# Kernel tuning notes

Measured on AMD Instinct MI355X. Metric: run time of the kernel, lower is better.

The kernel has to match this reference:

```python
import jax, jax.numpy as jnp
import numpy as np

NUM_HEADS = 16
HEAD_DIM = 128
EMBED = NUM_HEADS * HEAD_DIM  # 2048
BATCH, SEQ = 2, 2048


def setup_inputs() -> dict:
    key = jax.random.key(0)
    k1, k2 = jax.random.split(key)
    x = jax.random.normal(k1, (BATCH, SEQ, EMBED), dtype=jnp.float32)
    W = jax.random.normal(k2, (EMBED, 3 * EMBED), dtype=jnp.float32) * 0.02
    b = jnp.zeros((3 * EMBED,), dtype=jnp.float32)
    return {"x": x, "W": W, "b": b}


def _rotate_half(u):
    u1, u2 = jnp.split(u, 2, axis=-1)
    return jnp.concatenate([-u2, u1], axis=-1)


def reference(x, W, b):
    B, S, E = x.shape
    H, D = NUM_HEADS, HEAD_DIM
    # Fused QKV projection: [B,S,E] @ [E,3E] -> [B,S,3E]
    qkv = jnp.einsum('bse,ef->bsf', x, W) + b
    qkv = qkv.reshape(B, S, 3, H, D)
    q, k, v = qkv[:, :, 0], qkv[:, :, 1], qkv[:, :, 2]  # each [B,S,H,D]
    # Module's rotary embedding: sin/cos over arange(S*D), shared across heads
    t = jnp.arange(S * D, dtype=jnp.float32).reshape(1, S, 1, D)
    sin, cos = jnp.sin(t), jnp.cos(t)
    q = q * cos + _rotate_half(q) * sin
    k = k * cos + _rotate_half(k) * sin
    # Scaled dot-product attention over sequence, per head
    scale = 1.0 / jnp.sqrt(jnp.float32(D))
    attn = jnp.einsum('bqhd,bkhd->bhqk', q, k) * scale  # [B,H,S,S]
    w = jax.nn.softmax(attn, axis=-1)
    out = jnp.einsum('bhqk,bkhd->bqhd', w, v)  # [B,S,H,D]
    return out
```

## Files before the change

kernel.cpp:

```cpp
#include <hip/hip_runtime.h>
#include <stdint.h>

typedef unsigned short u16;
typedef __attribute__((ext_vector_type(8))) short bf16x8;
typedef __attribute__((ext_vector_type(4))) float f32x4;

#define NUM_B 2
#define SEQ   2048
#define SEQP  2080
#define NH    16
#define HD    128
#define EMB   2048
#define N3    6144
#define MM    4096
#define QT    256
#define WQ    32
#define KT    64
#define NTILE (SEQ / KT)

#define BM 128
#define BN 384
#define BK 64
#define NT_K (EMB / BK)

__device__ __forceinline__ u16 f2bf(float f) {
  union { float f; unsigned u; } c; c.f = f;
  return (u16)((c.u + 0x7FFFu + ((c.u >> 16) & 1u)) >> 16);
}
__device__ __forceinline__ void async16(const void* g, void* l) {
  __builtin_amdgcn_global_load_lds(
      (const __attribute__((address_space(1))) void*)g,
      (__attribute__((address_space(3))) void*)l, 16, 0, 0);
}

#define GBAR()   asm volatile("s_barrier" ::: "memory")
#define WLGKM0() asm volatile("s_waitcnt lgkmcnt(0)" ::: "memory")

#define CVT_BLKS (MM * EMB / 4 / 256)
#define TRN_BX   (N3 / 32)
__global__ void k_prep(const float* __restrict__ x, u16* __restrict__ xb,
                       float2* __restrict__ tab,
                       const float* __restrict__ W, u16* __restrict__ Wt) {
  __shared__ float t[32][33];
  const int bid = blockIdx.x;
  if (bid < CVT_BLKS) {
    int i = bid * 256 + threadIdx.x;
    const float4 v = ((const float4*)x)[i];
    ushort4 o;
    o.x = f2bf(v.x); o.y = f2bf(v.y); o.z = f2bf(v.z); o.w = f2bf(v.w);
    ((ushort4*)xb)[i] = o;
    if (i < SEQ * HD) {
      double tt = (double)i;
      tab[i] = make_float2((float)cos(tt), (float)sin(tt));
    }
  } else {
    int b2 = bid - CVT_BLKS;
    int n0 = (b2 % TRN_BX) * 32, k0 = (b2 / TRN_BX) * 32;
    int tx = threadIdx.x & 31, ty = threadIdx.x >> 5;
    #pragma unroll
    for (int i = ty; i < 32; i += 8)
      t[i][tx] = W[(size_t)(k0 + i) * N3 + n0 + tx];
    __syncthreads();
    #pragma unroll
    for (int i = ty; i < 32; i += 8)
      Wt[(size_t)(n0 + i) * EMB + k0 + tx] = f2bf(t[tx][i]);
  }
}

__global__ __launch_bounds__(512, 2) void k_gemm_qkv(
    const u16* __restrict__ xb, const u16* __restrict__ wt,
    const float* __restrict__ bias, const float2* __restrict__ tab,
    u16* __restrict__ qb, u16* __restrict__ kb, u16* __restrict__ vbt)
{
  __shared__ __align__(16) u16 lsA[2][BM * BK];
  __shared__ __align__(16) u16 lsB[2][BN * BK];
  const int tid = threadIdx.x;
  const int wave = tid >> 6, lane = tid & 63;
  const int lq = lane & 15, lr = lane >> 4;
  const int wr = wave >> 2, wc = wave & 3;
  const int m0 = blockIdx.y * BM, n0 = blockIdx.x * BN;

  auto stA = [&](int t) {
    const int kt = t * BK;
    #pragma unroll
    for (int ii = 0; ii < 2; ++ii) {
      int s = ii * 512 + tid;
      int row = s >> 3, gq = (s & 7) ^ (row & 7);
      async16(xb + (size_t)(m0 + row) * EMB + kt + gq * 8, &lsA[t & 1][s * 8]);
    }
  };
  auto stB = [&](int t, int u) {
    const int kt = t * BK;
    #pragma unroll
    for (int ii = 0; ii < 2; ++ii) {
      int s = u * 1024 + ii * 512 + tid;
      int row = s >> 3, gq = (s & 7) ^ (row & 7);
      async16(wt + (size_t)(n0 + row) * EMB + kt + gq * 8, &lsB[t & 1][s * 8]);
    }
  };

  f32x4 acc[4][6];
  #pragma unroll
  for (int i = 0; i < 4; ++i)
    #pragma unroll
    for (int j = 0; j < 6; ++j)
      acc[i][j] = f32x4{0.f, 0.f, 0.f, 0.f};

  int rbase[6];
  #pragma unroll
  for (int nf = 0; nf < 6; ++nf) {
    int pg = 3 * wc + (nf >> 1);
    int col = (pg >> 2) * 128 + (pg & 3) * 16 + (nf & 1) * 64 + lq;
    rbase[nf] = col * BK;
  }
  const int aRow0 = (wr * 64 + lq) * BK;
  int qsw[2];
  qsw[0] = ((0 + lr) ^ (lq & 7)) * 8;
  qsw[1] = ((4 + lr) ^ (lq & 7)) * 8;

  stA(0); stB(0, 0); stB(0, 1); stB(0, 2); stB(1, 0); stB(1, 1); stB(1, 2);
  asm volatile("s_waitcnt vmcnt(6)" ::: "memory");
  GBAR();

  for (int ti = 0; ti < NT_K / 2; ++ti) {
    const int t0 = 2 * ti, t1 = t0 + 1;
    const bool nl = (ti < NT_K / 2 - 1);

    #pragma unroll
    for (int hp = 0; hp < 2; ++hp) {
      const u16* Ap = lsA[hp];
      const u16* Bp = lsB[hp];
      bf16x8 bfr[6][2];

      #pragma unroll
      for (int ph = 0; ph < 2; ++ph) {
        if (ph == 0) {
          #pragma unroll
          for (int nf = 0; nf < 6; ++nf)
            #pragma unroll
            for (int kk = 0; kk < 2; ++kk)
              bfr[nf][kk] = *(const bf16x8*)(Bp + rbase[nf] + qsw[kk]);
        }
        bf16x8 af[2][2];
        #pragma unroll
        for (int mfl = 0; mfl < 2; ++mfl)
          #pragma unroll
          for (int kk = 0; kk < 2; ++kk)
            af[mfl][kk] = *(const bf16x8*)(Ap + aRow0 + ((ph * 2 + mfl) * 16) * BK + qsw[kk]);

        if (hp == 0) {
          if (ph == 0) {
            stA(t1);
          } else {
            if (nl) {
              stB(t0 + 2, 0); stB(t0 + 2, 1);
              asm volatile("s_waitcnt vmcnt(4)" ::: "memory");
            } else {
              asm volatile("s_waitcnt vmcnt(0)" ::: "memory");
            }
          }
        } else {
          if (ph == 0) {
            if (nl) { stA(t0 + 2); stB(t0 + 2, 2); }
          } else {
            if (nl) {
              stB(t1 + 2, 0); stB(t1 + 2, 1); stB(t1 + 2, 2);
              asm volatile("s_waitcnt vmcnt(6)" ::: "memory");
            }
          }
        }
        if (ph == 0) asm volatile("s_waitcnt lgkmcnt(8)" ::: "memory");

        GBAR();
        WLGKM0();
        __builtin_amdgcn_s_setprio(1);
        #pragma unroll
        for (int kk = 0; kk < 2; ++kk)
          #pragma unroll
          for (int mfl = 0; mfl < 2; ++mfl)
            #pragma unroll
            for (int nf = 0; nf < 6; ++nf)
              acc[ph * 2 + mfl][nf] = __builtin_amdgcn_mfma_f32_16x16x32_bf16(
                  af[mfl][kk], bfr[nf][kk], acc[ph * 2 + mfl][nf], 0, 0, 0);
        __builtin_amdgcn_s_setprio(0);
        GBAR();
      }
    }
  }

  const int m0w = m0 + wr * 64;
  const int bxH = n0 >> 7;
  #pragma unroll
  for (int pl = 0; pl < 3; ++pl) {
    const int pg = 3 * wc + pl;
    const int j = pg >> 2;
    const int s4 = pg & 3;
    const int H = bxH + j;
    const int w = H >> 4;
    const int h = H & 15;
    const int d1 = s4 * 16 + lq;
    const float b1 = bias[n0 + j * 128 + d1];
    const float b2 = bias[n0 + j * 128 + d1 + 64];

    if (w == 2) {
      #pragma unroll
      for (int mf = 0; mf < 4; ++mf) {
        int mg0 = m0w + mf * 16 + lr * 4;
        int b = mg0 >> 11, s0 = mg0 & 2047;
        ushort4 pk;
        pk.x = f2bf(acc[mf][2 * pl][0] + b1);
        pk.y = f2bf(acc[mf][2 * pl][1] + b1);
        pk.z = f2bf(acc[mf][2 * pl][2] + b1);
        pk.w = f2bf(acc[mf][2 * pl][3] + b1);
        *(ushort4*)(vbt + ((size_t)(b * NH + h) * HD + d1) * SEQP + s0) = pk;
        pk.x = f2bf(acc[mf][2 * pl + 1][0] + b2);
        pk.y = f2bf(acc[mf][2 * pl + 1][1] + b2);
        pk.z = f2bf(acc[mf][2 * pl + 1][2] + b2);
        pk.w = f2bf(acc[mf][2 * pl + 1][3] + b2);
        *(ushort4*)(vbt + ((size_t)(b * NH + h) * HD + d1 + 64) * SEQP + s0) = pk;
      }
    } else {
      u16* basep = (w == 0) ? qb : kb;
      const float qs = (w == 0) ? 0.12751569843736827f : 1.0f;
      #pragma unroll
      for (int mf = 0; mf < 4; ++mf)
        #pragma unroll
        for (int r = 0; r < 4; ++r) {
          int mg = m0w + mf * 16 + lr * 4 + r;
          int b = mg >> 11, s = mg & 2047;
          u16* dst = basep + ((size_t)(b * NH + h) * SEQ + s) * HD;
          float c1 = acc[mf][2 * pl][r]     + b1;
          float c2 = acc[mf][2 * pl + 1][r] + b2;
          float2 s1 = tab[s * HD + d1];
          float2 s2 = tab[s * HD + d1 + 64];
          dst[d1]      = f2bf((c1 * s1.x - c2 * s1.y) * qs);
          dst[d1 + 64] = f2bf((c2 * s2.x + c1 * s2.y) * qs);
        }
    }
  }
}

__global__ __launch_bounds__(512, 1) void k_flash(
    const u16* __restrict__ qb, const u16* __restrict__ kb,
    const u16* __restrict__ vbt, float* __restrict__ out)
{
  __shared__ __align__(16) u16 lsK[2][KT * HD];
  __shared__ __align__(16) u16 lsV[2][HD * KT];
  __shared__ __align__(16) u16 lsP[8][WQ * KT];

  const int tid = threadIdx.x;
  const int wave = tid >> 6, lane = tid & 63;
  const int lq = lane & 15, lr = lane >> 4;
  const int i = blockIdx.x;
  const int xcd = i & 7, j = i >> 3;
  const int bh = xcd * 4 + (j >> 3);
  const int q0 = (j & 7) * QT;
  const u16* Qg = qb + ((size_t)bh * SEQ + q0 + wave * WQ) * HD;
  const u16* Kg = kb + (size_t)bh * SEQ * HD;
  const u16* Vg = vbt + (size_t)bh * HD * SEQP;

  auto stage = [&](int tile, int buf) {
    const int k0 = tile * KT;
    #pragma unroll
    for (int ii = 0; ii < 2; ++ii) {
      int c = tid + ii * 512;
      int key = c >> 4, grp = c & 15;
      async16(Kg + (size_t)(k0 + key) * HD + ((grp ^ (key & 7)) * 8), lsK[buf] + c * 8);
    }
    #pragma unroll
    for (int ii = 0; ii < 2; ++ii) {
      int c = tid + ii * 512;
      int d = c >> 3, g2 = c & 7;
      async16(Vg + (size_t)d * SEQP + k0 + ((g2 ^ ((d >> 1) & 7)) * 8), lsV[buf] + c * 8);
    }
  };

  stage(0, 0);

  bf16x8 qf[2][4];
  #pragma unroll
  for (int qq = 0; qq < 2; ++qq)
    #pragma unroll
    for (int ks = 0; ks < 4; ++ks)
      qf[qq][ks] = *(const bf16x8*)(Qg + (size_t)(qq * 16 + lq) * HD + ks * 32 + lr * 8);

  f32x4 acc_o[2][8];
  float lsum[2] = {0.f, 0.f};
  #pragma unroll
  for (int mb = 0; mb < 2; ++mb)
    #pragma unroll
    for (int nb = 0; nb < 8; ++nb) acc_o[mb][nb] = f32x4{0.f, 0.f, 0.f, 0.f};

  for (int t = 0; t < NTILE; ++t) {
    const int p = t & 1;
    __syncthreads();
    if (t + 1 < NTILE) stage(t + 1, 1 - p);

    f32x4 sacc[4][2];
    #pragma unroll
    for (int kbi = 0; kbi < 4; ++kbi)
      #pragma unroll
      for (int qq = 0; qq < 2; ++qq) sacc[kbi][qq] = f32x4{0.f, 0.f, 0.f, 0.f};
    #pragma unroll
    for (int ks = 0; ks < 4; ++ks) {
      bf16x8 kf[4];
      #pragma unroll
      for (int kbi = 0; kbi < 4; ++kbi) {
        int key = kbi * 16 + lq;
        int g = (ks * 4 + lr) ^ (key & 7);
        kf[kbi] = *(const bf16x8*)(lsK[p] + key * HD + g * 8);
      }
      #pragma unroll
      for (int kbi = 0; kbi < 4; ++kbi)
        #pragma unroll
        for (int qq = 0; qq < 2; ++qq)
          sacc[kbi][qq] = __builtin_amdgcn_mfma_f32_16x16x32_bf16(kf[kbi], qf[qq][ks], sacc[kbi][qq], 0, 0, 0);
    }

    #pragma unroll
    for (int half = 0; half < 2; ++half) {
      #pragma unroll
      for (int kb2 = 0; kb2 < 2; ++kb2) {
        int kbi = half * 2 + kb2;
        #pragma unroll
        for (int qq = 0; qq < 2; ++qq) {
          float p0 = __builtin_amdgcn_exp2f(sacc[kbi][qq][0]);
          float p1 = __builtin_amdgcn_exp2f(sacc[kbi][qq][1]);
          float p2 = __builtin_amdgcn_exp2f(sacc[kbi][qq][2]);
          float p3 = __builtin_amdgcn_exp2f(sacc[kbi][qq][3]);
          lsum[qq] += (p0 + p1) + (p2 + p3);
          int row = qq * 16 + lq;
          int g = kbi * 4 + lr;
          int gp = g ^ (row & 6) ^ ((row & 8) >> 1);
          uint2 pk;
          pk.x = (uint32_t)f2bf(p0) | ((uint32_t)f2bf(p1) << 16);
          pk.y = (uint32_t)f2bf(p2) | ((uint32_t)f2bf(p3) << 16);
          *(uint2*)(lsP[wave] + row * KT + gp * 4) = pk;
        }
      }

      bf16x8 ap[2];
      #pragma unroll
      for (int mb = 0; mb < 2; ++mb) {
        int row = mb * 16 + lq;
        int sw = (row & 6) ^ ((row & 8) >> 1);
        int gb = (half * 8 + 2 * lr) ^ sw;
        ap[mb] = *(const bf16x8*)(lsP[wave] + row * KT + gb * 4);
      }
      #pragma unroll
      for (int nb = 0; nb < 8; ++nb) {
        int d = nb * 16 + lq;
        int q8 = (half * 4 + lr) ^ ((d >> 1) & 7);
        bf16x8 bv = *(const bf16x8*)(lsV[p] + d * KT + q8 * 8);
        #pragma unroll
        for (int mb = 0; mb < 2; ++mb)
          acc_o[mb][nb] = __builtin_amdgcn_mfma_f32_16x16x32_bf16(ap[mb], bv, acc_o[mb][nb], 0, 0, 0);
      }
    }
  }

  float inv[2];
  #pragma unroll
  for (int qq = 0; qq < 2; ++qq) {
    float s = lsum[qq];
    s += __shfl_xor(s, 16);
    s += __shfl_xor(s, 32);
    inv[qq] = 1.0f / s;
  }
  const int b = bh >> 4, h = bh & 15;
  #pragma unroll
  for (int mb = 0; mb < 2; ++mb)
    #pragma unroll
    for (int r = 0; r < 4; ++r) {
      float iv = __shfl(inv[mb], lr * 4 + r);
      int row = wave * WQ + mb * 16 + lr * 4 + r;
      int sq = q0 + row;
      float* op = out + (((size_t)b * SEQ + sq) * NH + h) * HD;
      #pragma unroll
      for (int nb = 0; nb < 8; ++nb)
        op[nb * 16 + lq] = acc_o[mb][nb][r] * iv;
    }
}


extern "C" void kernel_launch(void* const* d_in, const int* in_sizes, int n_in,
                              void* d_out, int out_size, void* d_ws, size_t ws_size,
                              hipStream_t stream) {
  (void)in_sizes; (void)n_in; (void)out_size; (void)ws_size;
  const float* x    = (const float*)d_in[0];
  const float* W    = (const float*)d_in[1];
  const float* bias = (const float*)d_in[2];
  float* out = (float*)d_out;

  char* p = (char*)d_ws;
  u16* xb  = (u16*)p;  p += (size_t)MM * EMB * 2;
  u16* wt  = (u16*)p;  p += (size_t)N3 * EMB * 2;
  u16* qb  = (u16*)p;  p += (size_t)NUM_B * NH * SEQ * HD * 2;
  u16* kb  = (u16*)p;  p += (size_t)NUM_B * NH * SEQ * HD * 2;
  u16* vbt = (u16*)p;  p += (size_t)NUM_B * NH * HD * SEQP * 2;
  float2* tab = (float2*)p;

  k_prep<<<CVT_BLKS + TRN_BX * (EMB / 32), 256, 0, stream>>>(x, xb, tab, W, wt);
  k_gemm_qkv<<<dim3(N3 / BN, MM / BM), 512, 0, stream>>>(xb, wt, bias, tab, qb, kb, vbt);
  k_flash<<<SEQ / QT * NUM_B * NH, 512, 0, stream>>>(qb, kb, vbt, out);
}
```

Before: 223.4 us.

## Shrink QKV GEMM tile to 128x128 with simple double-buffered loop

```diff
diff --git a/kernel.cpp b/kernel.cpp
--- a/kernel.cpp
+++ b/kernel.cpp
@@ -19,7 +19,7 @@
 #define NTILE (SEQ / KT)
 
 #define BM 128
-#define BN 384
+#define BN 128
 #define BK 64
 #define NT_K (EMB / BK)
 
@@ -34,7 +34,7 @@
 }
 
 #define GBAR()   asm volatile("s_barrier" ::: "memory")
-#define WLGKM0() asm volatile("s_waitcnt lgkmcnt(0)" ::: "memory")
+#define WVM0()   asm volatile("s_waitcnt vmcnt(0)" ::: "memory")
 
 #define CVT_BLKS (MM * EMB / 4 / 256)
 #define TRN_BX   (N3 / 32)
@@ -67,7 +67,7 @@
   }
 }
 
-__global__ __launch_bounds__(512, 2) void k_gemm_qkv(
+__global__ __launch_bounds__(256, 2) void k_gemm_qkv(
     const u16* __restrict__ xb, const u16* __restrict__ wt,
     const float* __restrict__ bias, const float2* __restrict__ tab,
     u16* __restrict__ qb, u16* __restrict__ kb, u16* __restrict__ vbt)
@@ -77,40 +77,38 @@
   const int tid = threadIdx.x;
   const int wave = tid >> 6, lane = tid & 63;
   const int lq = lane & 15, lr = lane >> 4;
-  const int wr = wave >> 2, wc = wave & 3;
+  const int wr = wave >> 1, wc = wave & 1;
   const int m0 = blockIdx.y * BM, n0 = blockIdx.x * BN;
 
-  auto stA = [&](int t) {
+  auto stage = [&](int t) {
     const int kt = t * BK;
-    #pragma unroll
-    for (int ii = 0; ii < 2; ++ii) {
-      int s = ii * 512 + tid;
+    const int buf = t & 1;
+    #pragma unroll
+    for (int ii = 0; ii < 4; ++ii) {
+      int s = ii * 256 + tid;
       int row = s >> 3, gq = (s & 7) ^ (row & 7);
-      async16(xb + (size_t)(m0 + row) * EMB + kt + gq * 8, &lsA[t & 1][s * 8]);
+      async16(xb + (size_t)(m0 + row) * EMB + kt + gq * 8, &lsA[buf][s * 8]);
+    }
+    #pragma unroll
+    for (int ii = 0; ii < 4; ++ii) {
+      int s = ii * 256 + tid;
+      int row = s >> 3, gq = (s & 7) ^ (row & 7);
+      async16(wt + (size_t)(n0 + row) * EMB + kt + gq * 8, &lsB[buf][s * 8]);
     }
   };
-  auto stB = [&](int t, int u) {
-    const int kt = t * BK;
-    #pragma unroll
-    for (int ii = 0; ii < 2; ++ii) {
-      int s = u * 1024 + ii * 512 + tid;
-      int row = s >> 3, gq = (s & 7) ^ (row & 7);
-      async16(wt + (size_t)(n0 + row) * EMB + kt + gq * 8, &lsB[t & 1][s * 8]);
-    }
-  };
-
-  f32x4 acc[4][6];
+
+  f32x4 acc[4][4];
   #pragma unroll
   for (int i = 0; i < 4; ++i)
     #pragma unroll
-    for (int j = 0; j < 6; ++j)
+    for (int j = 0; j < 4; ++j)
       acc[i][j] = f32x4{0.f, 0.f, 0.f, 0.f};
 
-  int rbase[6];
-  #pragma unroll
-  for (int nf = 0; nf < 6; ++nf) {
-    int pg = 3 * wc + (nf >> 1);
-    int col = (pg >> 2) * 128 + (pg & 3) * 16 + (nf & 1) * 64 + lq;
+  int rbase[4];
+  #pragma unroll
+  for (int nf = 0; nf < 4; ++nf) {
+    int half = nf & 1, pl = nf >> 1;
+    int col = half * 64 + wc * 32 + pl * 16 + lq;
     rbase[nf] = col * BK;
   }
   const int aRow0 = (wr * 64 + lq) * BK;
@@ -118,89 +116,48 @@
   qsw[0] = ((0 + lr) ^ (lq & 7)) * 8;
   qsw[1] = ((4 + lr) ^ (lq & 7)) * 8;
 
-  stA(0); stB(0, 0); stB(0, 1); stB(0, 2); stB(1, 0); stB(1, 1); stB(1, 2);
-  asm volatile("s_waitcnt vmcnt(6)" ::: "memory");
-  GBAR();
-
-  for (int ti = 0; ti < NT_K / 2; ++ti) {
-    const int t0 = 2 * ti, t1 = t0 + 1;
-    const bool nl = (ti < NT_K / 2 - 1);
-
-    #pragma unroll
-    for (int hp = 0; hp < 2; ++hp) {
-      const u16* Ap = lsA[hp];
-      const u16* Bp = lsB[hp];
-      bf16x8 bfr[6][2];
-
-      #pragma unroll
-      for (int ph = 0; ph < 2; ++ph) {
-        if (ph == 0) {
-          #pragma unroll
-          for (int nf = 0; nf < 6; ++nf)
-            #pragma unroll
-            for (int kk = 0; kk < 2; ++kk)
-              bfr[nf][kk] = *(const bf16x8*)(Bp + rbase[nf] + qsw[kk]);
-        }
-        bf16x8 af[2][2];
-        #pragma unroll
-        for (int mfl = 0; mfl < 2; ++mfl)
-          #pragma unroll
-          for (int kk = 0; kk < 2; ++kk)
-            af[mfl][kk] = *(const bf16x8*)(Ap + aRow0 + ((ph * 2 + mfl) * 16) * BK + qsw[kk]);
-
-        if (hp == 0) {
-          if (ph == 0) {
-            stA(t1);
-          } else {
-            if (nl) {
-              stB(t0 + 2, 0); stB(t0 + 2, 1);
-              asm volatile("s_waitcnt vmcnt(4)" ::: "memory");
-            } else {
-              asm volatile("s_waitcnt vmcnt(0)" ::: "memory");
-            }
-          }
-        } else {
-          if (ph == 0) {
-            if (nl) { stA(t0 + 2); stB(t0 + 2, 2); }
-          } else {
-            if (nl) {
-              stB(t1 + 2, 0); stB(t1 + 2, 1); stB(t1 + 2, 2);
-              asm volatile("s_waitcnt vmcnt(6)" ::: "memory");
-            }
-          }
-        }
-        if (ph == 0) asm volatile("s_waitcnt lgkmcnt(8)" ::: "memory");
-
-        GBAR();
-        WLGKM0();
-        __builtin_amdgcn_s_setprio(1);
-        #pragma unroll
-        for (int kk = 0; kk < 2; ++kk)
-          #pragma unroll
-          for (int mfl = 0; mfl < 2; ++mfl)
-            #pragma unroll
-            for (int nf = 0; nf < 6; ++nf)
-              acc[ph * 2 + mfl][nf] = __builtin_amdgcn_mfma_f32_16x16x32_bf16(
-                  af[mfl][kk], bfr[nf][kk], acc[ph * 2 + mfl][nf], 0, 0, 0);
-        __builtin_amdgcn_s_setprio(0);
-        GBAR();
-      }
+  stage(0);
+
+  for (int t = 0; t < NT_K; ++t) {
+    const int p = t & 1;
+    WVM0();
+    GBAR();
+    if (t + 1 < NT_K) stage(t + 1);
+
+    const u16* Ap = lsA[p];
+    const u16* Bp = lsB[p];
+
+    bf16x8 bfr[4][2];
+    #pragma unroll
+    for (int nf = 0; nf < 4; ++nf)
+      #pragma unroll
+      for (int kk = 0; kk < 2; ++kk)
+        bfr[nf][kk] = *(const bf16x8*)(Bp + rbase[nf] + qsw[kk]);
+
+    #pragma unroll
+    for (int mf = 0; mf < 4; ++mf) {
+      bf16x8 afk[2];
+      #pragma unroll
+      for (int kk = 0; kk < 2; ++kk)
+        afk[kk] = *(const bf16x8*)(Ap + aRow0 + (mf * 16) * BK + qsw[kk]);
+      #pragma unroll
+      for (int kk = 0; kk < 2; ++kk)
+        #pragma unroll
+        for (int nf = 0; nf < 4; ++nf)
+          acc[mf][nf] = __builtin_amdgcn_mfma_f32_16x16x32_bf16(
+              afk[kk], bfr[nf][kk], acc[mf][nf], 0, 0, 0);
     }
   }
 
   const int m0w = m0 + wr * 64;
-  const int bxH = n0 >> 7;
-  #pragma unroll
-  for (int pl = 0; pl < 3; ++pl) {
-    const int pg = 3 * wc + pl;
-    const int j = pg >> 2;
-    const int s4 = pg & 3;
-    const int H = bxH + j;
-    const int w = H >> 4;
-    const int h = H & 15;
-    const int d1 = s4 * 16 + lq;
-    const float b1 = bias[n0 + j * 128 + d1];
-    const float b2 = bias[n0 + j * 128 + d1 + 64];
+  const int H = blockIdx.x;
+  const int w = H >> 4;
+  const int h = H & 15;
+  #pragma unroll
+  for (int pl = 0; pl < 2; ++pl) {
+    const int d1 = wc * 32 + pl * 16 + lq;
+    const float b1 = bias[n0 + d1];
+    const float b2 = bias[n0 + d1 + 64];
 
     if (w == 2) {
       #pragma unroll
@@ -401,6 +358,6 @@
   float2* tab = (float2*)p;
 
   k_prep<<<CVT_BLKS + TRN_BX * (EMB / 32), 256, 0, stream>>>(x, xb, tab, W, wt);
-  k_gemm_qkv<<<dim3(N3 / BN, MM / BM), 512, 0, stream>>>(xb, wt, bias, tab, qb, kb, vbt);
+  k_gemm_qkv<<<dim3(N3 / BN, MM / BM), 256, 0, stream>>>(xb, wt, bias, tab, qb, kb, vbt);
   k_flash<<<SEQ / QT * NUM_B * NH, 512, 0, stream>>>(qb, kb, vbt, out);
 }
```

Measured after the change: 242.0 us. 8.3% more time.
